# Performance work log

Hardware: AMD Instinct MI355X
Metric: run time of the kernel (lower is better)

Reference implementation:

```python
import jax, jax.numpy as jnp
import numpy as np

# Dimensions (match init_kwargs)
B, N, D = 128, 256, 256   # batch, n_agents, obs_dim
MSG = 64                  # msg_dim
CD = 32                   # compressed_dim = int(msg_dim * 0.5)
K = 8                     # top-k recipients
H1, H2 = 128, 256         # msg_gen hidden, receiver hidden


def setup_inputs() -> dict:
    key = jax.random.key(0)
    ks = jax.random.split(key, 16)
    s = 0.02
    # All weights stored (in_features, out_features): y = x @ W + b
    return {
        "obs_all": jax.random.normal(ks[0], (B, N, D), dtype=jnp.float32),
        "W1": jax.random.normal(ks[1], (D, H1), dtype=jnp.float32) * s,
        "b1": jnp.zeros((H1,), jnp.float32),
        "W2": jax.random.normal(ks[2], (H1, MSG), dtype=jnp.float32) * s,
        "b2": jnp.zeros((MSG,), jnp.float32),
        "Wc": jax.random.normal(ks[3], (MSG, CD), dtype=jnp.float32) * s,
        "bc": jnp.zeros((CD,), jnp.float32),
        "Wd": jax.random.normal(ks[4], (CD, MSG), dtype=jnp.float32) * s,
        "bd": jnp.zeros((MSG,), jnp.float32),
        "Wbil": jax.random.normal(ks[5], (D, D), dtype=jnp.float32) * s,  # Bilinear weight (out=1)
        "bbil": jnp.zeros((), jnp.float32),
        "Wr1": jax.random.normal(ks[6], (D + MSG, H2), dtype=jnp.float32) * s,
        "br1": jnp.zeros((H2,), jnp.float32),
        "Wr2": jax.random.normal(ks[7], (H2, D), dtype=jnp.float32) * s,
        "br2": jnp.zeros((D,), jnp.float32),
    }


def reference(obs_all, W1, b1, W2, b2, Wc, bc, Wd, bd, Wbil, bbil, Wr1, br1, Wr2, br2):
    # send: msg_gen MLP -> compress -> decompress (all agents at once)
    h = jax.nn.relu(jnp.einsum('bnd,dh->bnh', obs_all, W1) + b1)
    full_msg = jnp.einsum('bnh,hm->bnm', h, W2) + b2          # (B, N, MSG)
    compressed = jnp.einsum('bnm,mc->bnc', full_msg, Wc) + bc  # (B, N, CD)
    msgs = jnp.einsum('bnc,cm->bnm', compressed, Wd) + bd      # (B, N, MSG)

    # pairwise bilinear relevance: scores[b,i,j] = obs_i^T Wbil obs_j + bias
    tmp = jnp.einsum('bid,de->bie', obs_all, Wbil)
    scores = jnp.einsum('bie,bje->bij', tmp, obs_all) + bbil   # (B, N, N)

    # top-k gating: softmax over the k selected scores, zeros elsewhere
    topk_vals, topk_idx = jax.lax.top_k(scores, K)             # (B, N, K)
    gate_vals = jax.nn.softmax(topk_vals, axis=-1)             # (B, N, K)

    # weighted aggregation of selected messages (honor top-k sparsity:
    # gather the K messages per receiver instead of building dense gates)
    sel_msgs = jax.vmap(lambda m, ix: m[ix])(msgs, topk_idx)   # (B, N, K, MSG)
    agg = jnp.einsum('bik,bikm->bim', gate_vals, sel_msgs)     # (B, N, MSG)

    # receive: MLP over [obs, aggregated message]
    combined = jnp.concatenate([obs_all, agg], axis=-1)        # (B, N, D+MSG)
    r = jax.nn.relu(jnp.einsum('bnc,ch->bnh', combined, Wr1) + br1)
    enriched = jnp.einsum('bnh,hd->bnd', r, Wr2) + br2          # (B, N, D)
    return enriched
```

## Files before the change

### kernel.cpp

```cpp
#include <hip/hip_runtime.h>
#include <cstddef>

#define BB   128
#define NN   256
#define DIMD 256
#define MSG  64
#define CDIM 32
#define TOPK 8
#define H1D  128
#define H2D  256
#define BN   (BB*NN)

typedef unsigned short u16;
typedef u16   u16x4  __attribute__((ext_vector_type(4)));
typedef u16   u16x8  __attribute__((ext_vector_type(8)));
typedef short short8 __attribute__((ext_vector_type(8)));
typedef float f32x4  __attribute__((ext_vector_type(4)));

__device__ __forceinline__ u16 f2bf(float f) {
    return (u16)((__float_as_uint(f) + 0x8000u) >> 16);
}
__device__ __forceinline__ float bf2f(u16 u) {
    return __uint_as_float(((unsigned)u) << 16);
}
#define MFMA16(a,b,c) __builtin_amdgcn_mfma_f32_16x16x32_bf16((a),(b),(c),0,0,0)


__global__ __launch_bounds__(256) void prep_w_k(
    const float* __restrict__ W1, const float* __restrict__ W2,
    const float* __restrict__ Wc, const float* __restrict__ Wd,
    const float* __restrict__ Wb, const float* __restrict__ Wr1,
    const float* __restrict__ Wr2,
    u16* __restrict__ Wp1, u16* __restrict__ Wp2, u16* __restrict__ Wpc,
    u16* __restrict__ Wpd, u16* __restrict__ WpB, u16* __restrict__ Wpr1,
    u16* __restrict__ Wpr2)
{
    const int t = blockIdx.x * 256 + threadIdx.x;
    const float* src; u16* dst; int I, os, loc;
    if      (t <  32768) { src = W1;  dst = Wp1;  I = 256; os = 7; loc = t; }
    else if (t <  40960) { src = W2;  dst = Wp2;  I = 128; os = 6; loc = t - 32768; }
    else if (t <  43008) { src = Wc;  dst = Wpc;  I = 64;  os = 5; loc = t - 40960; }
    else if (t <  45056) { src = Wd;  dst = Wpd;  I = 32;  os = 6; loc = t - 43008; }
    else if (t < 110592) { src = Wb;  dst = WpB;  I = 256; os = 8; loc = t - 45056; }
    else if (t < 192512) { src = Wr1; dst = Wpr1; I = 320; os = 8; loc = t - 110592; }
    else                 { src = Wr2; dst = Wpr2; I = 256; os = 8; loc = t - 192512; }
    const int i = loc >> os;
    const int o = loc & ((1 << os) - 1);
    const int nt = o >> 4, ls = o & 15;
    const int KB = I >> 5;
    const int kk = i >> 5, q = (i & 31) >> 3, j = i & 7;
    dst[((size_t)(nt*KB + kk)*64 + q*16 + ls)*8 + j] = f2bf(src[loc]);
}

__global__ __launch_bounds__(256) __attribute__((amdgpu_waves_per_eu(4, 4)))
void sendpack_k(
    const float* __restrict__ obs, u16* __restrict__ obs_p,
    const u16* __restrict__ Wp1, const float* __restrict__ b1,
    const u16* __restrict__ Wp2, const float* __restrict__ b2,
    const u16* __restrict__ Wpc, const float* __restrict__ bc,
    const u16* __restrict__ Wpd, const float* __restrict__ bd,
    u16* __restrict__ msgs_bf)
{
    __shared__ __align__(16) u16 sO[32][264];
    __shared__ __align__(16) u16 sH[32][136];
    __shared__ __align__(16) u16 sF[32][72];
    __shared__ __align__(16) u16 sC[32][40];
    const int t = threadIdx.x;
    const int w = t >> 6, l = t & 63, q = l >> 4, ls = l & 15;
    const int row0 = blockIdx.x * 32;
    const int tile0 = blockIdx.x * 2;

    {
        const float4* src = (const float4*)(obs + (size_t)row0 * 256);
        #pragma unroll
        for (int i = 0; i < 8; ++i) {
            const int idx = t + 256*i;
            const int r = idx >> 6, c4 = idx & 63;
            const float4 v = src[idx];
            u16x4 o;
            o[0] = f2bf(v.x); o[1] = f2bf(v.y); o[2] = f2bf(v.z); o[3] = f2bf(v.w);
            *(u16x4*)&sO[r][c4*4] = o;
        }
    }
    __syncthreads();
    {
        #pragma unroll
        for (int i = 0; i < 4; ++i) {
            const int u = t + 256*i;
            const int tile = u >> 9, kk = (u >> 6) & 7, lane = u & 63;
            const u16x8 v = *(const u16x8*)&sO[tile*16 + (lane & 15)][kk*32 + (lane >> 4)*8];
            *(u16x8*)(obs_p + (size_t)(tile0 + tile)*4096 + (size_t)(kk*64 + lane)*8) = v;
        }
    }
    {
        f32x4 acc[2][2];
        #pragma unroll
        for (int mi = 0; mi < 2; ++mi)
            #pragma unroll
            for (int nn = 0; nn < 2; ++nn) acc[mi][nn] = (f32x4){0,0,0,0};
        short8 cb[2];
        #pragma unroll
        for (int nn = 0; nn < 2; ++nn)
            cb[nn] = *(const short8*)(Wp1 + ((size_t)((w*2+nn)*8))*512 + l*8);
        #pragma unroll
        for (int kk = 0; kk < 8; ++kk) {
            short8 nb[2];
            if (kk < 7) {
                #pragma unroll
                for (int nn = 0; nn < 2; ++nn)
                    nb[nn] = *(const short8*)(Wp1 + ((size_t)((w*2+nn)*8 + kk+1))*512 + l*8);
            }
            short8 a[2];
            a[0] = *(const short8*)&sO[ls][kk*32 + q*8];
            a[1] = *(const short8*)&sO[16 + ls][kk*32 + q*8];
            #pragma unroll
            for (int mi = 0; mi < 2; ++mi)
                #pragma unroll
                for (int nn = 0; nn < 2; ++nn)
                    acc[mi][nn] = MFMA16(a[mi], cb[nn], acc[mi][nn]);
            if (kk < 7) {
                #pragma unroll
                for (int nn = 0; nn < 2; ++nn) cb[nn] = nb[nn];
            }
        }
        #pragma unroll
        for (int nn = 0; nn < 2; ++nn) {
            const float bv = b1[(w*2+nn)*16 + ls];
            #pragma unroll
            for (int mi = 0; mi < 2; ++mi)
                #pragma unroll
                for (int r = 0; r < 4; ++r)
                    sH[mi*16 + q*4 + r][(w*2+nn)*16 + ls] = f2bf(fmaxf(acc[mi][nn][r] + bv, 0.0f));
        }
    }
    __syncthreads();
    {
        f32x4 acc[2];
        acc[0] = (f32x4){0,0,0,0}; acc[1] = (f32x4){0,0,0,0};
        #pragma unroll
        for (int kk = 0; kk < 4; ++kk) {
            const int k0 = kk * 32;
            short8 a[2];
            a[0] = *(const short8*)(&sH[ls][k0 + q*8]);
            a[1] = *(const short8*)(&sH[16 + ls][k0 + q*8]);
            const short8 bf = *(const short8*)(Wp2 + ((size_t)(w*4 + kk)*64 + l)*8);
            acc[0] = MFMA16(a[0], bf, acc[0]);
            acc[1] = MFMA16(a[1], bf, acc[1]);
        }
        const float bv = b2[w*16 + ls];
        #pragma unroll
        for (int mi = 0; mi < 2; ++mi)
            #pragma unroll
            for (int r = 0; r < 4; ++r)
                sF[mi*16 + q*4 + r][w*16 + ls] = f2bf(acc[mi][r] + bv);
    }
    __syncthreads();
    if (w < 2) {
        f32x4 acc[2];
        acc[0] = (f32x4){0,0,0,0}; acc[1] = (f32x4){0,0,0,0};
        #pragma unroll
        for (int kk = 0; kk < 2; ++kk) {
            const int k0 = kk * 32;
            short8 a[2];
            a[0] = *(const short8*)(&sF[ls][k0 + q*8]);
            a[1] = *(const short8*)(&sF[16 + ls][k0 + q*8]);
            const short8 bf = *(const short8*)(Wpc + ((size_t)(w*2 + kk)*64 + l)*8);
            acc[0] = MFMA16(a[0], bf, acc[0]);
            acc[1] = MFMA16(a[1], bf, acc[1]);
        }
        const float bv = bc[w*16 + ls];
        #pragma unroll
        for (int mi = 0; mi < 2; ++mi)
            #pragma unroll
            for (int r = 0; r < 4; ++r)
                sC[mi*16 + q*4 + r][w*16 + ls] = f2bf(acc[mi][r] + bv);
    }
    __syncthreads();
    {
        f32x4 acc[2];
        acc[0] = (f32x4){0,0,0,0}; acc[1] = (f32x4){0,0,0,0};
        short8 a[2];
        a[0] = *(const short8*)(&sC[ls][q*8]);
        a[1] = *(const short8*)(&sC[16 + ls][q*8]);
        const short8 bf = *(const short8*)(Wpd + ((size_t)w*64 + l)*8);
        acc[0] = MFMA16(a[0], bf, acc[0]);
        acc[1] = MFMA16(a[1], bf, acc[1]);
        const float bv = bd[w*16 + ls];
        #pragma unroll
        for (int mi = 0; mi < 2; ++mi)
            #pragma unroll
            for (int r = 0; r < 4; ++r)
                msgs_bf[(size_t)(row0 + mi*16 + q*4 + r)*MSG + w*16 + ls] = f2bf(acc[mi][r] + bv);
    }
}

__global__ __launch_bounds__(256) __attribute__((amdgpu_waves_per_eu(4, 4)))
void relrecv_k(
    const u16* __restrict__ obs_p, const u16* __restrict__ WpB,
    const float* __restrict__ bbil, const u16* __restrict__ msgs_bf,
    const u16* __restrict__ Wpr1, const float* __restrict__ br1,
    const u16* __restrict__ Wpr2, const float* __restrict__ br2,
    float* __restrict__ out)
{
    __shared__ __align__(16) u16 sS[32][264];
    __shared__ __align__(16) u16 sA[32][72];
    __shared__ float sG[32][8];
    __shared__ unsigned short sI[32][8];
    const int t = threadIdx.x;
    const int w = t >> 6, l = t & 63, q = l >> 4, ls = l & 15;
    const int bid = blockIdx.x;
    const int xcd = bid & 7, idx = bid >> 3;
    const int b   = xcd * 16 + (idx >> 3);
    const int mc  = idx & 7;
    const int row0g = b * NN + mc * 32;
    const int mt0   = b * 16 + mc * 2;

    {
        f32x4 acc[2][4];
        #pragma unroll
        for (int mi = 0; mi < 2; ++mi)
            #pragma unroll
            for (int nn = 0; nn < 4; ++nn) acc[mi][nn] = (f32x4){0,0,0,0};
        short8 ca[2], cb[4];
        #pragma unroll
        for (int mi = 0; mi < 2; ++mi)
            ca[mi] = *(const short8*)(obs_p + ((size_t)((mt0+mi)*8))*512 + l*8);
        #pragma unroll
        for (int nn = 0; nn < 4; ++nn)
            cb[nn] = *(const short8*)(WpB + ((size_t)((w*4+nn)*8))*512 + l*8);
        #pragma unroll
        for (int kk = 0; kk < 8; ++kk) {
            short8 na[2], nb[4];
            if (kk < 7) {
                #pragma unroll
                for (int mi = 0; mi < 2; ++mi)
                    na[mi] = *(const short8*)(obs_p + ((size_t)((mt0+mi)*8 + kk+1))*512 + l*8);
                #pragma unroll
                for (int nn = 0; nn < 4; ++nn)
                    nb[nn] = *(const short8*)(WpB + ((size_t)((w*4+nn)*8 + kk+1))*512 + l*8);
            }
            #pragma unroll
            for (int mi = 0; mi < 2; ++mi)
                #pragma unroll
                for (int nn = 0; nn < 4; ++nn)
                    acc[mi][nn] = MFMA16(ca[mi], cb[nn], acc[mi][nn]);
            if (kk < 7) {
                #pragma unroll
                for (int mi = 0; mi < 2; ++mi) ca[mi] = na[mi];
                #pragma unroll
                for (int nn = 0; nn < 4; ++nn) cb[nn] = nb[nn];
            }
        }
        #pragma unroll
        for (int mi = 0; mi < 2; ++mi)
            #pragma unroll
            for (int nn = 0; nn < 4; ++nn)
                #pragma unroll
                for (int r = 0; r < 4; ++r)
                    sS[mi*16 + q*4 + r][(w*4+nn)*16 + ls] = f2bf(acc[mi][nn][r]);
    }
    __syncthreads();
    {
        const float bb = bbil[0];
        f32x4 acc[2][4];
        #pragma unroll
        for (int mi = 0; mi < 2; ++mi)
            #pragma unroll
            for (int nn = 0; nn < 4; ++nn) acc[mi][nn] = (f32x4){0,0,0,0};
        short8 cb[4];
        #pragma unroll
        for (int nn = 0; nn < 4; ++nn)
            cb[nn] = *(const short8*)(obs_p + ((size_t)((b*16 + w*4+nn)*8))*512 + l*8);
        #pragma unroll
        for (int kk = 0; kk < 8; ++kk) {
            short8 nb[4];
            if (kk < 7) {
                #pragma unroll
                for (int nn = 0; nn < 4; ++nn)
                    nb[nn] = *(const short8*)(obs_p + ((size_t)((b*16 + w*4+nn)*8 + kk+1))*512 + l*8);
            }
            const int k0 = kk * 32;
            short8 a[2];
            a[0] = *(const short8*)(&sS[ls][k0 + q*8]);
            a[1] = *(const short8*)(&sS[16 + ls][k0 + q*8]);
            #pragma unroll
            for (int mi = 0; mi < 2; ++mi)
                #pragma unroll
                for (int nn = 0; nn < 4; ++nn)
                    acc[mi][nn] = MFMA16(a[mi], cb[nn], acc[mi][nn]);
            if (kk < 7) {
                #pragma unroll
                for (int nn = 0; nn < 4; ++nn) cb[nn] = nb[nn];
            }
        }
        __syncthreads();
        #pragma unroll
        for (int mi = 0; mi < 2; ++mi)
            #pragma unroll
            for (int nn = 0; nn < 4; ++nn)
                #pragma unroll
                for (int r = 0; r < 4; ++r)
                    sS[mi*16 + q*4 + r][(w*4+nn)*16 + ls] = f2bf(acc[mi][nn][r] + bb);
    }
    __syncthreads();
    {
        const int r = t >> 3, g = t & 7;
        u16 buf[32];
        #pragma unroll
        for (int c = 0; c < 4; ++c)
            *(u16x8*)&buf[c*8] = *(const u16x8*)&sS[r][g*32 + c*8];
        float val[8]; int idx8[8];
        #pragma unroll
        for (int j = 0; j < 8; ++j) { val[j] = -3.4028235e38f; idx8[j] = 1 << 30; }
        #pragma unroll
        for (int i = 0; i < 32; ++i) {
            const int   id = g*32 + i;
            const float v  = bf2f(buf[i]);
            if (v > val[7]) {
                #pragma unroll
                for (int j = 7; j >= 1; --j) {
                    const bool cj  = v > val[j];
                    const bool cjm = v > val[j-1];
                    val[j]  = cj ? (cjm ? val[j-1]  : v ) : val[j];
                    idx8[j] = cj ? (cjm ? idx8[j-1] : id) : idx8[j];
                }
                const bool c0 = v > val[0];
                val[0]  = c0 ? v  : val[0];
                idx8[0] = c0 ? id : idx8[0];
            }
        }
        float wv[8]; int wi[8];
        #pragma unroll
        for (int k = 0; k < 8; ++k) {
            float hv = val[0]; int hi = idx8[0];
            float ov; int oi;
            ov = __shfl_xor(hv, 1); oi = __shfl_xor(hi, 1);
            if (ov > hv || (ov == hv && oi < hi)) { hv = ov; hi = oi; }
            ov = __shfl_xor(hv, 2); oi = __shfl_xor(hi, 2);
            if (ov > hv || (ov == hv && oi < hi)) { hv = ov; hi = oi; }
            ov = __shfl_xor(hv, 4); oi = __shfl_xor(hi, 4);
            if (ov > hv || (ov == hv && oi < hi)) { hv = ov; hi = oi; }
            wv[k] = hv; wi[k] = hi;
            const bool won = (val[0] == hv) && (idx8[0] == hi);
            #pragma unroll
            for (int j = 0; j < 7; ++j) {
                val[j]  = won ? val[j+1]  : val[j];
                idx8[j] = won ? idx8[j+1] : idx8[j];
            }
            val[7]  = won ? -3.4028235e38f : val[7];
            idx8[7] = won ? (1 << 30)      : idx8[7];
        }
        if (g == 0) {
            float e[8]; float s = 0.0f;
            #pragma unroll
            for (int k = 0; k < 8; ++k) { e[k] = __expf(wv[k] - wv[0]); s += e[k]; }
            const float inv = 1.0f / s;
            #pragma unroll
            for (int k = 0; k < 8; ++k) {
                sG[r][k] = e[k] * inv;
                sI[r][k] = (unsigned short)wi[k];
            }
        }
    }
    {
        for (int rr = 0; rr < 8; ++rr) {
            const int row = w*8 + rr;
            float a = 0.0f;
            #pragma unroll
            for (int k = 0; k < 8; ++k) {
                const float gt = sG[row][k];
                const int   id = sI[row][k];
                a = fmaf(gt, bf2f(msgs_bf[((size_t)b*NN + id)*MSG + l]), a);
            }
            sA[row][l] = f2bf(a);
        }
    }
    __syncthreads();
    {
        f32x4 acc[2][4];
        #pragma unroll
        for (int mi = 0; mi < 2; ++mi)
            #pragma unroll
            for (int nn = 0; nn < 4; ++nn) acc[mi][nn] = (f32x4){0,0,0,0};
        short8 ca[2], cb[4];
        #pragma unroll
        for (int mi = 0; mi < 2; ++mi)
            ca[mi] = *(const short8*)(obs_p + ((size_t)((mt0+mi)*8))*512 + l*8);
        #pragma unroll
        for (int nn = 0; nn < 4; ++nn)
            cb[nn] = *(const short8*)(Wpr1 + ((size_t)((w*4+nn)*10))*512 + l*8);
        #pragma unroll
        for (int kk = 0; kk < 10; ++kk) {
            short8 na[2], nb[4];
            if (kk < 9) {
                if (kk < 7) {
                    #pragma unroll
                    for (int mi = 0; mi < 2; ++mi)
                        na[mi] = *(const short8*)(obs_p + ((size_t)((mt0+mi)*8 + kk+1))*512 + l*8);
                } else {
                    #pragma unroll
                    for (int mi = 0; mi < 2; ++mi)
                        na[mi] = *(const short8*)&sA[mi*16 + ls][(kk+1-8)*32 + q*8];
                }
                #pragma unroll
                for (int nn = 0; nn < 4; ++nn)
                    nb[nn] = *(const short8*)(Wpr1 + ((size_t)((w*4+nn)*10 + kk+1))*512 + l*8);
            }
            #pragma unroll
            for (int mi = 0; mi < 2; ++mi)
                #pragma unroll
                for (int nn = 0; nn < 4; ++nn)
                    acc[mi][nn] = MFMA16(ca[mi], cb[nn], acc[mi][nn]);
            if (kk < 9) {
                #pragma unroll
                for (int mi = 0; mi < 2; ++mi) ca[mi] = na[mi];
                #pragma unroll
                for (int nn = 0; nn < 4; ++nn) cb[nn] = nb[nn];
            }
        }
        __syncthreads();
        #pragma unroll
        for (int nn = 0; nn < 4; ++nn) {
            const float bv = br1[(w*4+nn)*16 + ls];
            #pragma unroll
            for (int mi = 0; mi < 2; ++mi)
                #pragma unroll
                for (int r = 0; r < 4; ++r)
                    sS[mi*16 + q*4 + r][(w*4+nn)*16 + ls] = f2bf(fmaxf(acc[mi][nn][r] + bv, 0.0f));
        }
    }
    __syncthreads();
    {
        f32x4 acc[2][4];
        #pragma unroll
        for (int mi = 0; mi < 2; ++mi)
            #pragma unroll
            for (int nn = 0; nn < 4; ++nn) acc[mi][nn] = (f32x4){0,0,0,0};
        short8 cb[4];
        #pragma unroll
        for (int nn = 0; nn < 4; ++nn)
            cb[nn] = *(const short8*)(Wpr2 + ((size_t)((w*4+nn)*8))*512 + l*8);
        #pragma unroll
        for (int kk = 0; kk < 8; ++kk) {
            short8 nb[4];
            if (kk < 7) {
                #pragma unroll
                for (int nn = 0; nn < 4; ++nn)
                    nb[nn] = *(const short8*)(Wpr2 + ((size_t)((w*4+nn)*8 + kk+1))*512 + l*8);
            }
            const int k0 = kk * 32;
            short8 a[2];
            a[0] = *(const short8*)(&sS[ls][k0 + q*8]);
            a[1] = *(const short8*)(&sS[16 + ls][k0 + q*8]);
            #pragma unroll
            for (int mi = 0; mi < 2; ++mi)
                #pragma unroll
                for (int nn = 0; nn < 4; ++nn)
                    acc[mi][nn] = MFMA16(a[mi], cb[nn], acc[mi][nn]);
            if (kk < 7) {
                #pragma unroll
                for (int nn = 0; nn < 4; ++nn) cb[nn] = nb[nn];
            }
        }
        #pragma unroll
        for (int nn = 0; nn < 4; ++nn) {
            const float bv = br2[(w*4+nn)*16 + ls];
            #pragma unroll
            for (int mi = 0; mi < 2; ++mi)
                #pragma unroll
                for (int r = 0; r < 4; ++r)
                    out[(size_t)(row0g + mi*16 + q*4 + r)*DIMD + (w*4+nn)*16 + ls] = acc[mi][nn][r] + bv;
        }
    }
}

extern "C" void kernel_launch(void* const* d_in, const int* in_sizes, int n_in,
                              void* d_out, int out_size, void* d_ws, size_t ws_size,
                              hipStream_t stream)
{
    (void)in_sizes; (void)n_in; (void)out_size; (void)ws_size;
    const float* obs  = (const float*)d_in[0];
    const float* W1   = (const float*)d_in[1];
    const float* b1   = (const float*)d_in[2];
    const float* W2   = (const float*)d_in[3];
    const float* b2   = (const float*)d_in[4];
    const float* Wc   = (const float*)d_in[5];
    const float* bc   = (const float*)d_in[6];
    const float* Wd   = (const float*)d_in[7];
    const float* bd   = (const float*)d_in[8];
    const float* Wbil = (const float*)d_in[9];
    const float* bbil = (const float*)d_in[10];
    const float* Wr1  = (const float*)d_in[11];
    const float* br1  = (const float*)d_in[12];
    const float* Wr2  = (const float*)d_in[13];
    const float* br2  = (const float*)d_in[14];
    float* outp = (float*)d_out;

    u16* obs_p   = (u16*)d_ws;
    u16* msgs_bf = obs_p   + (size_t)BN*256;
    u16* Wp1  = msgs_bf + (size_t)BN*64;
    u16* Wp2  = Wp1  + 32768;
    u16* Wpc  = Wp2  + 8192;
    u16* Wpd  = Wpc  + 2048;
    u16* WpB  = Wpd  + 2048;
    u16* Wpr1 = WpB  + 65536;
    u16* Wpr2 = Wpr1 + 81920;

    prep_w_k<<<1008, 256, 0, stream>>>(W1, W2, Wc, Wd, Wbil, Wr1, Wr2,
                                       Wp1, Wp2, Wpc, Wpd, WpB, Wpr1, Wpr2);
    sendpack_k<<<BN/32, 256, 0, stream>>>(obs, obs_p, Wp1, b1, Wp2, b2,
                                          Wpc, bc, Wpd, bd, msgs_bf);
    relrecv_k<<<BN/32, 256, 0, stream>>>(obs_p, WpB, bbil, msgs_bf,
                                         Wpr1, br1, Wpr2, br2, outp);
}
```

Before: 59.79 us.

## Stage obs tile in LDS and triple-buffer weight prefetch across GEMM stages

Each block's 32-row obs tile is loaded into shared memory once and reused by both the bilinear-projection GEMM and the receiver's first GEMM, so it is no longer read twice from global memory. B-operand fragments now use a three-deep register ring with prefetch distance two, and the first fragments of each following GEMM are issued before the preceding barrier or gather so they overlap it. The message gather issues all eight indexed loads before the FMAs. This adds 16 KB of LDS and more live registers under a fixed four-waves-per-EU bound, which could cause spills.

```diff
diff --git a/kernel.cpp b/kernel.cpp
--- a/kernel.cpp
+++ b/kernel.cpp
@@ -204,6 +204,7 @@
 {
     __shared__ __align__(16) u16 sS[32][264];
     __shared__ __align__(16) u16 sA[32][72];
+    __shared__ __align__(16) u16 sObs[8192];
     __shared__ float sG[32][8];
     __shared__ unsigned short sI[32][8];
     const int t = threadIdx.x;
@@ -215,41 +216,42 @@
     const int row0g = b * NN + mc * 32;
     const int mt0   = b * 16 + mc * 2;
 
+    short8 pb[3][4];
+
+    {
+        const u16x8* src = (const u16x8*)(obs_p + (size_t)mt0 * 4096);
+        #pragma unroll
+        for (int i = 0; i < 4; ++i)
+            *(u16x8*)&sObs[(t + 256*i) * 8] = src[t + 256*i];
+    }
+    #pragma unroll
+    for (int d = 0; d < 2; ++d)
+        #pragma unroll
+        for (int nn = 0; nn < 4; ++nn)
+            pb[d][nn] = *(const short8*)(WpB + ((size_t)((w*4+nn)*8 + d))*512 + l*8);
+    __syncthreads();
+
     {
         f32x4 acc[2][4];
         #pragma unroll
         for (int mi = 0; mi < 2; ++mi)
             #pragma unroll
             for (int nn = 0; nn < 4; ++nn) acc[mi][nn] = (f32x4){0,0,0,0};
-        short8 ca[2], cb[4];
-        #pragma unroll
-        for (int mi = 0; mi < 2; ++mi)
-            ca[mi] = *(const short8*)(obs_p + ((size_t)((mt0+mi)*8))*512 + l*8);
-        #pragma unroll
-        for (int nn = 0; nn < 4; ++nn)
-            cb[nn] = *(const short8*)(WpB + ((size_t)((w*4+nn)*8))*512 + l*8);
         #pragma unroll
         for (int kk = 0; kk < 8; ++kk) {
-            short8 na[2], nb[4];
-            if (kk < 7) {
-                #pragma unroll
-                for (int mi = 0; mi < 2; ++mi)
-                    na[mi] = *(const short8*)(obs_p + ((size_t)((mt0+mi)*8 + kk+1))*512 + l*8);
-                #pragma unroll
-                for (int nn = 0; nn < 4; ++nn)
-                    nb[nn] = *(const short8*)(WpB + ((size_t)((w*4+nn)*8 + kk+1))*512 + l*8);
-            }
-            #pragma unroll
-            for (int mi = 0; mi < 2; ++mi)
-                #pragma unroll
-                for (int nn = 0; nn < 4; ++nn)
-                    acc[mi][nn] = MFMA16(ca[mi], cb[nn], acc[mi][nn]);
-            if (kk < 7) {
-                #pragma unroll
-                for (int mi = 0; mi < 2; ++mi) ca[mi] = na[mi];
-                #pragma unroll
-                for (int nn = 0; nn < 4; ++nn) cb[nn] = nb[nn];
-            }
+            if (kk < 6) {
+                #pragma unroll
+                for (int nn = 0; nn < 4; ++nn)
+                    pb[(kk+2)%3][nn] = *(const short8*)(WpB + ((size_t)((w*4+nn)*8 + kk+2))*512 + l*8);
+            }
+            short8 a[2];
+            a[0] = *(const short8*)&sObs[0*4096 + kk*512 + l*8];
+            a[1] = *(const short8*)&sObs[1*4096 + kk*512 + l*8];
+            #pragma unroll
+            for (int mi = 0; mi < 2; ++mi)
+                #pragma unroll
+                for (int nn = 0; nn < 4; ++nn)
+                    acc[mi][nn] = MFMA16(a[mi], pb[kk%3][nn], acc[mi][nn]);
         }
         #pragma unroll
         for (int mi = 0; mi < 2; ++mi)
@@ -259,7 +261,13 @@
                 for (int r = 0; r < 4; ++r)
                     sS[mi*16 + q*4 + r][(w*4+nn)*16 + ls] = f2bf(acc[mi][nn][r]);
     }
-    __syncthreads();
+    #pragma unroll
+    for (int d = 0; d < 2; ++d)
+        #pragma unroll
+        for (int nn = 0; nn < 4; ++nn)
+            pb[d][nn] = *(const short8*)(obs_p + ((size_t)((b*16 + w*4+nn)*8 + d))*512 + l*8);
+    __syncthreads();
+
     {
         const float bb = bbil[0];
         f32x4 acc[2][4];
@@ -267,17 +275,12 @@
         for (int mi = 0; mi < 2; ++mi)
             #pragma unroll
             for (int nn = 0; nn < 4; ++nn) acc[mi][nn] = (f32x4){0,0,0,0};
-        short8 cb[4];
-        #pragma unroll
-        for (int nn = 0; nn < 4; ++nn)
-            cb[nn] = *(const short8*)(obs_p + ((size_t)((b*16 + w*4+nn)*8))*512 + l*8);
         #pragma unroll
         for (int kk = 0; kk < 8; ++kk) {
-            short8 nb[4];
-            if (kk < 7) {
-                #pragma unroll
-                for (int nn = 0; nn < 4; ++nn)
-                    nb[nn] = *(const short8*)(obs_p + ((size_t)((b*16 + w*4+nn)*8 + kk+1))*512 + l*8);
+            if (kk < 6) {
+                #pragma unroll
+                for (int nn = 0; nn < 4; ++nn)
+                    pb[(kk+2)%3][nn] = *(const short8*)(obs_p + ((size_t)((b*16 + w*4+nn)*8 + kk+2))*512 + l*8);
             }
             const int k0 = kk * 32;
             short8 a[2];
@@ -287,11 +290,7 @@
             for (int mi = 0; mi < 2; ++mi)
                 #pragma unroll
                 for (int nn = 0; nn < 4; ++nn)
-                    acc[mi][nn] = MFMA16(a[mi], cb[nn], acc[mi][nn]);
-            if (kk < 7) {
-                #pragma unroll
-                for (int nn = 0; nn < 4; ++nn) cb[nn] = nb[nn];
-            }
+                    acc[mi][nn] = MFMA16(a[mi], pb[kk%3][nn], acc[mi][nn]);
         }
         __syncthreads();
         #pragma unroll
@@ -362,16 +361,24 @@
             }
         }
     }
-    {
+    #pragma unroll
+    for (int d = 0; d < 2; ++d)
+        #pragma unroll
+        for (int nn = 0; nn < 4; ++nn)
+            pb[d][nn] = *(const short8*)(Wpr1 + ((size_t)((w*4+nn)*10 + d))*512 + l*8);
+    {
+        const u16* mb = msgs_bf + (size_t)b*NN*MSG + l;
+        #pragma unroll
         for (int rr = 0; rr < 8; ++rr) {
             const int row = w*8 + rr;
+            u16 mv[8];
+            #pragma unroll
+            for (int k = 0; k < 8; ++k)
+                mv[k] = mb[(size_t)sI[row][k]*MSG];
             float a = 0.0f;
             #pragma unroll
-            for (int k = 0; k < 8; ++k) {
-                const float gt = sG[row][k];
-                const int   id = sI[row][k];
-                a = fmaf(gt, bf2f(msgs_bf[((size_t)b*NN + id)*MSG + l]), a);
-            }
+            for (int k = 0; k < 8; ++k)
+                a = fmaf(sG[row][k], bf2f(mv[k]), a);
             sA[row][l] = f2bf(a);
         }
     }
@@ -382,42 +389,32 @@
         for (int mi = 0; mi < 2; ++mi)
             #pragma unroll
             for (int nn = 0; nn < 4; ++nn) acc[mi][nn] = (f32x4){0,0,0,0};
-        short8 ca[2], cb[4];
-        #pragma unroll
-        for (int mi = 0; mi < 2; ++mi)
-            ca[mi] = *(const short8*)(obs_p + ((size_t)((mt0+mi)*8))*512 + l*8);
-        #pragma unroll
-        for (int nn = 0; nn < 4; ++nn)
-            cb[nn] = *(const short8*)(Wpr1 + ((size_t)((w*4+nn)*10))*512 + l*8);
         #pragma unroll
         for (int kk = 0; kk < 10; ++kk) {
-            short8 na[2], nb[4];
-            if (kk < 9) {
-                if (kk < 7) {
-                    #pragma unroll
-                    for (int mi = 0; mi < 2; ++mi)
-                        na[mi] = *(const short8*)(obs_p + ((size_t)((mt0+mi)*8 + kk+1))*512 + l*8);
-                } else {
-                    #pragma unroll
-                    for (int mi = 0; mi < 2; ++mi)
-                        na[mi] = *(const short8*)&sA[mi*16 + ls][(kk+1-8)*32 + q*8];
-                }
-                #pragma unroll
-                for (int nn = 0; nn < 4; ++nn)
-                    nb[nn] = *(const short8*)(Wpr1 + ((size_t)((w*4+nn)*10 + kk+1))*512 + l*8);
-            }
-            #pragma unroll
-            for (int mi = 0; mi < 2; ++mi)
-                #pragma unroll
-                for (int nn = 0; nn < 4; ++nn)
-                    acc[mi][nn] = MFMA16(ca[mi], cb[nn], acc[mi][nn]);
-            if (kk < 9) {
-                #pragma unroll
-                for (int mi = 0; mi < 2; ++mi) ca[mi] = na[mi];
-                #pragma unroll
-                for (int nn = 0; nn < 4; ++nn) cb[nn] = nb[nn];
-            }
-        }
+            if (kk < 8) {
+                #pragma unroll
+                for (int nn = 0; nn < 4; ++nn)
+                    pb[(kk+2)%3][nn] = *(const short8*)(Wpr1 + ((size_t)((w*4+nn)*10 + kk+2))*512 + l*8);
+            }
+            short8 a[2];
+            if (kk < 8) {
+                a[0] = *(const short8*)&sObs[0*4096 + kk*512 + l*8];
+                a[1] = *(const short8*)&sObs[1*4096 + kk*512 + l*8];
+            } else {
+                a[0] = *(const short8*)&sA[0*16 + ls][(kk-8)*32 + q*8];
+                a[1] = *(const short8*)&sA[16 + ls][(kk-8)*32 + q*8];
+            }
+            #pragma unroll
+            for (int mi = 0; mi < 2; ++mi)
+                #pragma unroll
+                for (int nn = 0; nn < 4; ++nn)
+                    acc[mi][nn] = MFMA16(a[mi], pb[kk%3][nn], acc[mi][nn]);
+        }
+        #pragma unroll
+        for (int d = 0; d < 2; ++d)
+            #pragma unroll
+            for (int nn = 0; nn < 4; ++nn)
+                pb[d][nn] = *(const short8*)(Wpr2 + ((size_t)((w*4+nn)*8 + d))*512 + l*8);
         __syncthreads();
         #pragma unroll
         for (int nn = 0; nn < 4; ++nn) {
@@ -436,17 +433,12 @@
         for (int mi = 0; mi < 2; ++mi)
             #pragma unroll
             for (int nn = 0; nn < 4; ++nn) acc[mi][nn] = (f32x4){0,0,0,0};
-        short8 cb[4];
-        #pragma unroll
-        for (int nn = 0; nn < 4; ++nn)
-            cb[nn] = *(const short8*)(Wpr2 + ((size_t)((w*4+nn)*8))*512 + l*8);
         #pragma unroll
         for (int kk = 0; kk < 8; ++kk) {
-            short8 nb[4];
-            if (kk < 7) {
-                #pragma unroll
-                for (int nn = 0; nn < 4; ++nn)
-                    nb[nn] = *(const short8*)(Wpr2 + ((size_t)((w*4+nn)*8 + kk+1))*512 + l*8);
+            if (kk < 6) {
+                #pragma unroll
+                for (int nn = 0; nn < 4; ++nn)
+                    pb[(kk+2)%3][nn] = *(const short8*)(Wpr2 + ((size_t)((w*4+nn)*8 + kk+2))*512 + l*8);
             }
             const int k0 = kk * 32;
             short8 a[2];
@@ -456,11 +448,7 @@
             for (int mi = 0; mi < 2; ++mi)
                 #pragma unroll
                 for (int nn = 0; nn < 4; ++nn)
-                    acc[mi][nn] = MFMA16(a[mi], cb[nn], acc[mi][nn]);
-            if (kk < 7) {
-                #pragma unroll
-                for (int nn = 0; nn < 4; ++nn) cb[nn] = nb[nn];
-            }
+                    acc[mi][nn] = MFMA16(a[mi], pb[kk%3][nn], acc[mi][nn]);
         }
         #pragma unroll
         for (int nn = 0; nn < 4; ++nn) {
```

Result: faster. 58.28 us (-2.5%).
